# Performance work log

Measured on AMD Instinct MI355X. Metric: run time of the kernel, lower is better.

Reference implementation:

```python
import jax, jax.numpy as jnp
import numpy as np

S, B, H = 2048, 2, 2048
NH = 16
HD = H // NH
SCALE = HD ** -0.5


def setup_inputs() -> dict:
    key = jax.random.key(0)
    ks = jax.random.split(key, 5)
    sigma = 0.02
    return {
        "x": jax.random.normal(ks[0], (S, B, H), dtype=jnp.float32),
        "wq": jax.random.normal(ks[1], (H, H), dtype=jnp.float32) * sigma,
        "wk": jax.random.normal(ks[2], (H, H), dtype=jnp.float32) * sigma,
        "wv": jax.random.normal(ks[3], (H, H), dtype=jnp.float32) * sigma,
        "wo": jax.random.normal(ks[4], (H, H), dtype=jnp.float32) * sigma,
    }


def reference(x, wq, wk, wv, wo):
    # x: [s, b, h]; F.linear(x, W) == x @ W.T
    q = x @ wq.T
    k = x @ wk.T
    v = x @ wv.T
    s, b, _ = q.shape
    # [s, b, h] -> [b, nh, s, hd]
    def split_heads(t):
        return t.reshape(s, b, NH, HD).transpose(1, 2, 0, 3)
    q, k, v = split_heads(q), split_heads(k), split_heads(v)
    scores = jnp.einsum("bhqd,bhkd->bhqk", q, k) * SCALE
    attn = jax.nn.softmax(scores.astype(jnp.float32), axis=-1).astype(q.dtype)
    out = jnp.einsum("bhqk,bhkd->bhqd", attn, v)
    # [b, nh, s, hd] -> [s, b, h]
    out = out.transpose(2, 0, 1, 3).reshape(s, b, NH * HD)
    return out @ wo.T
```

## Files before the change

### kernel.cpp

```cpp
#include <hip/hip_runtime.h>

typedef __bf16 bf16;
typedef __bf16 bf16x8 __attribute__((ext_vector_type(8)));
typedef float f32x4 __attribute__((ext_vector_type(4)));
typedef float f32x16 __attribute__((ext_vector_type(16)));
typedef unsigned int uint;

#define GLOAD16(g, l)                                                        \
  __builtin_amdgcn_global_load_lds(                                          \
      (const __attribute__((address_space(1))) void*)(g),                    \
      (__attribute__((address_space(3))) void*)(l), 16, 0, 0)

__device__ inline uint pack_bf16(float a, float b) {
  union { bf16 h[2]; uint u; } x;
  x.h[0] = (bf16)a; x.h[1] = (bf16)b;
  return x.u;
}

__global__ void cast_f32_to_bf16(const float* __restrict__ in,
                                 bf16* __restrict__ out, int n8, float scale) {
  int i = blockIdx.x * blockDim.x + threadIdx.x;
  if (i >= n8) return;
  const float4* p = reinterpret_cast<const float4*>(in) + (size_t)i * 2;
  float4 a = p[0], b = p[1];
  bf16x8 o;
  o[0] = (bf16)(a.x * scale); o[1] = (bf16)(a.y * scale);
  o[2] = (bf16)(a.z * scale); o[3] = (bf16)(a.w * scale);
  o[4] = (bf16)(b.x * scale); o[5] = (bf16)(b.y * scale);
  o[6] = (bf16)(b.z * scale); o[7] = (bf16)(b.w * scale);
  *reinterpret_cast<bf16x8*>(out + (size_t)i * 8) = o;
}

template <typename OT>
__global__ __launch_bounds__(512, 2) void gemm_nt_256(
    const bf16* __restrict__ A, const bf16* __restrict__ B, OT* __restrict__ C,
    int K, int lda, int ldb, int ldc, long bsB, long bsC) {
  extern __shared__ char sh[];
  const int t = threadIdx.x;
  const int w = t >> 6, lane = t & 63;
  const int l15 = lane & 15, l4 = lane >> 4;
  const int wr = w >> 1, wc = w & 1;
  const int m0 = blockIdx.y * 256;
  const int n0 = blockIdx.x * 128;
  const bf16* Bg = B + (size_t)blockIdx.z * bsB;
  OT* Cg = C + (size_t)blockIdx.z * bsC;

  int sRow[4], sCol[4];
#pragma unroll
  for (int i = 0; i < 4; i++) {
    int sB_ = (i * 512 + t) * 16;
    int row = sB_ >> 7;
    int ge = (sB_ ^ ((row & 7) << 4)) >> 1;
    sRow[i] = ge >> 6;
    sCol[i] = ge & 63;
  }

  const int NT = K >> 6;
  f32x4 acc[4][4] = {};

  auto stage = [&](int tt) {
    char* dst = sh + (size_t)(tt % 3) * 49152;
    const int k0 = tt * 64;
#pragma unroll
    for (int i = 0; i < 4; i++)
      GLOAD16(A + (size_t)(m0 + sRow[i]) * lda + k0 + sCol[i],
              dst + (i * 512 + w * 64) * 16);
#pragma unroll
    for (int i = 0; i < 2; i++)
      GLOAD16(Bg + (size_t)(n0 + sRow[i]) * ldb + k0 + sCol[i],
              dst + 32768 + (i * 512 + w * 64) * 16);
  };

  auto compute = [&](int tt) {
    const char* Ab = sh + (size_t)(tt % 3) * 49152;
    const char* Bb = Ab + 32768;
    bf16x8 bfr[4][2];
#pragma unroll
    for (int n = 0; n < 4; n++)
#pragma unroll
      for (int kk = 0; kk < 2; kk++) {
        int row = wc * 64 + n * 16 + l15;
        int off = (row * 128 + kk * 64 + l4 * 16) ^ ((row & 7) << 4);
        bfr[n][kk] = *reinterpret_cast<const bf16x8*>(Bb + off);
      }
#pragma unroll
    for (int mh = 0; mh < 2; mh++) {
      bf16x8 af[2][2];
#pragma unroll
      for (int m = 0; m < 2; m++)
#pragma unroll
        for (int kk = 0; kk < 2; kk++) {
          int row = wr * 64 + (mh * 2 + m) * 16 + l15;
          int off = (row * 128 + kk * 64 + l4 * 16) ^ ((row & 7) << 4);
          af[m][kk] = *reinterpret_cast<const bf16x8*>(Ab + off);
        }
      __builtin_amdgcn_s_setprio(1);
#pragma unroll
      for (int m = 0; m < 2; m++)
#pragma unroll
        for (int n = 0; n < 4; n++)
#pragma unroll
          for (int kk = 0; kk < 2; kk++)
            acc[mh * 2 + m][n] = __builtin_amdgcn_mfma_f32_16x16x32_bf16(
                af[m][kk], bfr[n][kk], acc[mh * 2 + m][n], 0, 0, 0);
      __builtin_amdgcn_s_setprio(0);
    }
  };

  stage(0);
  stage(1);
  for (int tt = 0; tt < NT - 1; ++tt) {
    asm volatile("s_waitcnt vmcnt(6)" ::: "memory");
    __builtin_amdgcn_s_barrier();
    if (tt + 2 < NT) stage(tt + 2);
    compute(tt);
  }
  asm volatile("s_waitcnt vmcnt(0)" ::: "memory");
  __builtin_amdgcn_s_barrier();
  compute(NT - 1);

#pragma unroll
  for (int m = 0; m < 4; m++)
#pragma unroll
    for (int n = 0; n < 4; n++)
#pragma unroll
      for (int j = 0; j < 4; j++) {
        int row = m0 + wr * 64 + m * 16 + l4 * 4 + j;
        int col = n0 + wc * 64 + n * 16 + l15;
        Cg[(size_t)row * ldc + col] = (OT)acc[m][n][j];
      }
}

__global__ __launch_bounds__(512, 2) void attn_fwd(
    const bf16* __restrict__ Q, const bf16* __restrict__ Kb,
    const bf16* __restrict__ Vt, bf16* __restrict__ O) {
  __shared__ bf16 Ks[2][64 * 128];
  __shared__ bf16 Vs[2][128 * 64];
  const int t = threadIdx.x, w = t >> 6, lane = t & 63;
  const int l31 = lane & 31, half = lane >> 5;
  const int bh = blockIdx.x;
  const int b = bh >> 4, h = bh & 15;
  const int sq0 = blockIdx.y * 256 + w * 32;
  const size_t hoff = (size_t)h * 128;
  const size_t bO = (size_t)b * 2048 + hoff;

  bf16x8 qf[8];
  {
    const bf16* qp = Q + ((size_t)(sq0 + l31) * 2 + b) * 2048 + hoff + half * 8;
#pragma unroll
    for (int dc = 0; dc < 8; dc++)
      qf[dc] = *reinterpret_cast<const bf16x8*>(qp + dc * 16);
  }

  f32x16 acc_o[4] = {};
  float m_run = -3e38f, l_run = 0.f;

  auto stage = [&](int nb, int sk0) {
#pragma unroll
    for (int i = 0; i < 2; i++) {
      int sB = (i * 512 + t) * 16;
      int row = sB >> 8;
      int ge = (sB ^ ((row & 7) << 4)) >> 1;
      GLOAD16(Kb + ((size_t)(sk0 + (ge >> 7)) * 2 + b) * 2048 + hoff + (ge & 127),
              Ks[nb] + (i * 512 + w * 64) * 8);
    }
#pragma unroll
    for (int i = 0; i < 2; i++) {
      int sB = (i * 512 + t) * 16;
      int row = sB >> 7;
      int ge = (sB ^ ((row & 7) << 4)) >> 1;
      GLOAD16(Vt + (bO + (ge >> 6)) * 2048 + sk0 + (ge & 63),
              Vs[nb] + (i * 512 + w * 64) * 8);
    }
  };

  stage(0, 0);

  for (int it = 0; it < 32; ++it) {
    const int cur = it & 1;
    __syncthreads();
    if (it + 1 < 32) stage(cur ^ 1, (it + 1) * 64);

    const char* ksb = reinterpret_cast<const char*>(Ks[cur]);
    const char* vsb = reinterpret_cast<const char*>(Vs[cur]);

    f32x16 sc[2] = {};
    __builtin_amdgcn_s_setprio(1);
#pragma unroll
    for (int dc = 0; dc < 8; dc++) {
#pragma unroll
      for (int kt = 0; kt < 2; kt++) {
        int kB = (((kt * 32 + l31) << 8) + dc * 32 + half * 16) ^ ((l31 & 7) << 4);
        bf16x8 kf = *reinterpret_cast<const bf16x8*>(ksb + kB);
        sc[kt] = __builtin_amdgcn_mfma_f32_32x32x16_bf16(kf, qf[dc], sc[kt], 0, 0, 0);
      }
    }
    __builtin_amdgcn_s_setprio(0);

    float pmax = -3e38f;
#pragma unroll
    for (int kt = 0; kt < 2; kt++)
#pragma unroll
      for (int r = 0; r < 16; r++) pmax = fmaxf(pmax, sc[kt][r]);
    pmax = fmaxf(pmax, __shfl_xor(pmax, 32));

    if (!__all(pmax - m_run <= 11.0f)) {
      float mn = fmaxf(m_run, pmax);
      float f = exp2f(m_run - mn);
      m_run = mn;
      l_run *= f;
#pragma unroll
      for (int idx = 0; idx < 16; idx++) {
        float fr = __shfl(f, (idx & 3) + 8 * (idx >> 2) + half * 4);
#pragma unroll
        for (int dcb = 0; dcb < 4; dcb++) acc_o[dcb][idx] *= fr;
      }
    }

    float rs = 0.f;
#pragma unroll
    for (int kt = 0; kt < 2; kt++)
#pragma unroll
      for (int r = 0; r < 16; r++) {
        float p = exp2f(sc[kt][r] - m_run);
        sc[kt][r] = p;
        rs += p;
      }
    rs += __shfl_xor(rs, 32);
    l_run += rs;

    uint pa[4][4];
#pragma unroll
    for (int skc = 0; skc < 4; skc++) {
      int kt = skc >> 1, s8 = (skc & 1) * 8;
      uint pk01 = pack_bf16(sc[kt][s8 + 0], sc[kt][s8 + 1]);
      uint pk23 = pack_bf16(sc[kt][s8 + 2], sc[kt][s8 + 3]);
      uint pk45 = pack_bf16(sc[kt][s8 + 4], sc[kt][s8 + 5]);
      uint pk67 = pack_bf16(sc[kt][s8 + 6], sc[kt][s8 + 7]);
      uint o01 = __shfl_xor(pk01, 32), o23 = __shfl_xor(pk23, 32);
      uint o45 = __shfl_xor(pk45, 32), o67 = __shfl_xor(pk67, 32);
      pa[skc][0] = half ? o45 : pk01;
      pa[skc][1] = half ? o67 : pk23;
      pa[skc][2] = half ? pk45 : o01;
      pa[skc][3] = half ? pk67 : o23;
    }

    __builtin_amdgcn_s_setprio(1);
#pragma unroll
    for (int dcb = 0; dcb < 4; dcb++) {
#pragma unroll
      for (int skc = 0; skc < 4; skc++) {
        int vB = (((dcb * 32 + l31) << 7) + skc * 32 + half * 16) ^ ((l31 & 7) << 4);
        bf16x8 vf = *reinterpret_cast<const bf16x8*>(vsb + vB);
        union { uint u[4]; bf16x8 v; } af;
        af.u[0] = pa[skc][0]; af.u[1] = pa[skc][1];
        af.u[2] = pa[skc][2]; af.u[3] = pa[skc][3];
        acc_o[dcb] = __builtin_amdgcn_mfma_f32_32x32x16_bf16(af.v, vf, acc_o[dcb], 0, 0, 0);
      }
    }
    __builtin_amdgcn_s_setprio(0);
  }

  float inv = 1.0f / l_run;
#pragma unroll
  for (int idx = 0; idx < 16; idx++) {
    int sr = (idx & 3) + 8 * (idx >> 2) + half * 4;
    float invr = __shfl(inv, sr);
    bf16* op = O + ((size_t)(sq0 + sr) * 2 + b) * 2048 + hoff + l31;
#pragma unroll
    for (int dcb = 0; dcb < 4; dcb++)
      op[dcb * 32] = (bf16)(acc_o[dcb][idx] * invr);
  }
}

extern "C" void kernel_launch(void* const* d_in, const int* in_sizes, int n_in,
                              void* d_out, int out_size, void* d_ws,
                              size_t ws_size, hipStream_t stream) {
  (void)in_sizes; (void)n_in; (void)out_size; (void)ws_size;
  const float* x  = (const float*)d_in[0];
  const float* wq = (const float*)d_in[1];
  const float* wk = (const float*)d_in[2];
  const float* wv = (const float*)d_in[3];
  const float* wo = (const float*)d_in[4];
  float* out = (float*)d_out;
  char* ws = (char*)d_ws;
  bf16* xb   = (bf16*)(ws);
  bf16* qb   = (bf16*)(ws + (1u << 24));
  bf16* kb   = (bf16*)(ws + (2u << 24));
  bf16* vt   = (bf16*)(ws + (3u << 24));
  bf16* wb   = (bf16*)(ws + (4u << 24));
  bf16* attn = xb;
  const float SCALE = 0.08838834764831845f * 1.4426950408889634f;
  const int SMEM = 3 * 49152;

  hipFuncSetAttribute((const void*)gemm_nt_256<bf16>,
                      hipFuncAttributeMaxDynamicSharedMemorySize, SMEM);
  hipFuncSetAttribute((const void*)gemm_nt_256<float>,
                      hipFuncAttributeMaxDynamicSharedMemorySize, SMEM);

  cast_f32_to_bf16<<<4096, 256, 0, stream>>>(x, xb, 8388608 / 8, 1.0f);

  dim3 g1(16, 16, 1);
  cast_f32_to_bf16<<<2048, 256, 0, stream>>>(wq, wb, 4194304 / 8, SCALE);
  gemm_nt_256<bf16><<<g1, 512, SMEM, stream>>>(xb, wb, qb, 2048, 2048, 2048, 2048, 0, 0);

  cast_f32_to_bf16<<<2048, 256, 0, stream>>>(wk, wb, 4194304 / 8, 1.0f);
  gemm_nt_256<bf16><<<g1, 512, SMEM, stream>>>(xb, wb, kb, 2048, 2048, 2048, 2048, 0, 0);

  cast_f32_to_bf16<<<2048, 256, 0, stream>>>(wv, wb, 4194304 / 8, 1.0f);
  dim3 g2(16, 8, 2);
  gemm_nt_256<bf16><<<g2, 512, SMEM, stream>>>(wb, xb, vt, 2048, 2048, 4096, 2048,
                                               2048L, 4194304L);

  dim3 ga(32, 8);
  attn_fwd<<<ga, 512, 0, stream>>>(qb, kb, vt, attn);

  cast_f32_to_bf16<<<2048, 256, 0, stream>>>(wo, wb, 4194304 / 8, 1.0f);
  gemm_nt_256<float><<<g1, 512, SMEM, stream>>>(attn, wb, out, 2048, 2048, 2048, 2048, 0, 0);
}
```

Before: 278.5 us.

## Shrink attention blocks to 4 waves and redesign LDS swizzle with precomputed load pointers

The attention kernel now uses 256-thread blocks covering 128 query rows, launched on twice as many blocks along the query axis. The K/V LDS tiles use a new 16-way XOR swizzle, with V stored as 64 rows of 256 bytes. Global-to-LDS source pointers are precomputed once outside the loop instead of being recomputed per stage. Each block now amortizes its K/V staging over fewer query rows, in exchange for more blocks and a possible change in occupancy and bank-conflict behaviour.

```diff
diff --git a/kernel.cpp b/kernel.cpp
--- a/kernel.cpp
+++ b/kernel.cpp
@@ -131,16 +131,16 @@
       }
 }
 
-__global__ __launch_bounds__(512, 2) void attn_fwd(
+__global__ __launch_bounds__(256, 2) void attn_fwd(
     const bf16* __restrict__ Q, const bf16* __restrict__ Kb,
     const bf16* __restrict__ Vt, bf16* __restrict__ O) {
   __shared__ bf16 Ks[2][64 * 128];
-  __shared__ bf16 Vs[2][128 * 64];
+  __shared__ bf16 Vs[2][64 * 128];
   const int t = threadIdx.x, w = t >> 6, lane = t & 63;
   const int l31 = lane & 31, half = lane >> 5;
   const int bh = blockIdx.x;
   const int b = bh >> 4, h = bh & 15;
-  const int sq0 = blockIdx.y * 256 + w * 32;
+  const int sq0 = blockIdx.y * 128 + w * 32;
   const size_t hoff = (size_t)h * 128;
   const size_t bO = (size_t)b * 2048 + hoff;
 
@@ -152,27 +152,29 @@
       qf[dc] = *reinterpret_cast<const bf16x8*>(qp + dc * 16);
   }
 
+  const bf16* kp[4];
+  const bf16* vp[4];
+#pragma unroll
+  for (int i = 0; i < 4; i++) {
+    int s = i * 256 + t;
+    int row = s >> 4, g = s & 15;
+    int lg = g ^ (row & 15);
+    kp[i] = Kb + ((size_t)row * 2 + b) * 2048 + hoff + lg * 8;
+    int d = row * 2 + (lg >> 3);
+    vp[i] = Vt + (bO + d) * 2048 + (lg & 7) * 8;
+  }
+
+  auto stage = [&](int nb, int sk0) {
+#pragma unroll
+    for (int i = 0; i < 4; i++)
+      GLOAD16(kp[i] + (size_t)sk0 * 4096, Ks[nb] + (i * 256 + w * 64) * 8);
+#pragma unroll
+    for (int i = 0; i < 4; i++)
+      GLOAD16(vp[i] + sk0, Vs[nb] + (i * 256 + w * 64) * 8);
+  };
+
   f32x16 acc_o[4] = {};
   float m_run = -3e38f, l_run = 0.f;
-
-  auto stage = [&](int nb, int sk0) {
-#pragma unroll
-    for (int i = 0; i < 2; i++) {
-      int sB = (i * 512 + t) * 16;
-      int row = sB >> 8;
-      int ge = (sB ^ ((row & 7) << 4)) >> 1;
-      GLOAD16(Kb + ((size_t)(sk0 + (ge >> 7)) * 2 + b) * 2048 + hoff + (ge & 127),
-              Ks[nb] + (i * 512 + w * 64) * 8);
-    }
-#pragma unroll
-    for (int i = 0; i < 2; i++) {
-      int sB = (i * 512 + t) * 16;
-      int row = sB >> 7;
-      int ge = (sB ^ ((row & 7) << 4)) >> 1;
-      GLOAD16(Vt + (bO + (ge >> 6)) * 2048 + sk0 + (ge & 63),
-              Vs[nb] + (i * 512 + w * 64) * 8);
-    }
-  };
 
   stage(0, 0);
 
@@ -188,9 +190,10 @@
     __builtin_amdgcn_s_setprio(1);
 #pragma unroll
     for (int dc = 0; dc < 8; dc++) {
+      int kx = ((dc * 2 + half) ^ (l31 & 15)) << 4;
 #pragma unroll
       for (int kt = 0; kt < 2; kt++) {
-        int kB = (((kt * 32 + l31) << 8) + dc * 32 + half * 16) ^ ((l31 & 7) << 4);
+        int kB = ((kt * 32 + l31) << 8) + kx;
         bf16x8 kf = *reinterpret_cast<const bf16x8*>(ksb + kB);
         sc[kt] = __builtin_amdgcn_mfma_f32_32x32x16_bf16(kf, qf[dc], sc[kt], 0, 0, 0);
       }
@@ -248,9 +251,11 @@
     __builtin_amdgcn_s_setprio(1);
 #pragma unroll
     for (int dcb = 0; dcb < 4; dcb++) {
+      int rp = dcb * 16 + (l31 >> 1);
+      int pbit = (l31 & 1) << 3;
 #pragma unroll
       for (int skc = 0; skc < 4; skc++) {
-        int vB = (((dcb * 32 + l31) << 7) + skc * 32 + half * 16) ^ ((l31 & 7) << 4);
+        int vB = (rp << 8) + (((pbit + skc * 2 + half) ^ (l31 >> 1)) << 4);
         bf16x8 vf = *reinterpret_cast<const bf16x8*>(vsb + vB);
         union { uint u[4]; bf16x8 v; } af;
         af.u[0] = pa[skc][0]; af.u[1] = pa[skc][1];
@@ -312,8 +317,8 @@
   gemm_nt_256<bf16><<<g2, 512, SMEM, stream>>>(wb, xb, vt, 2048, 2048, 4096, 2048,
                                                2048L, 4194304L);
 
-  dim3 ga(32, 8);
-  attn_fwd<<<ga, 512, 0, stream>>>(qb, kb, vt, attn);
+  dim3 ga(32, 16);
+  attn_fwd<<<ga, 256, 0, stream>>>(qb, kb, vt, attn);
 
   cast_f32_to_bf16<<<2048, 256, 0, stream>>>(wo, wb, 4194304 / 8, 1.0f);
   gemm_nt_256<float><<<g1, 512, SMEM, stream>>>(attn, wb, out, 2048, 2048, 2048, 2048, 0, 0);
```

Result: faster. 272.7 us (-2.1%).
